# Kernel tuning notes

Hardware: AMD Instinct MI355X
Metric: run time of the kernel (lower is better)

The kernel has to match this reference:

```python
import jax, jax.numpy as jnp
import numpy as np

N_NODES = 100000
N_EDGES = 1600000
D_FEAT = 48


def setup_inputs() -> dict:
    key = jax.random.key(0)
    k1, k2, k3, k4 = jax.random.split(key, 4)
    rows = jax.random.randint(k1, (N_EDGES,), 0, N_NODES, dtype=jnp.int32)
    cols = jax.random.randint(k2, (N_EDGES,), 0, N_NODES, dtype=jnp.int32)
    vals = jax.random.uniform(k3, (N_EDGES,), dtype=jnp.float32)
    embeds = jax.random.normal(k4, (N_NODES, D_FEAT), dtype=jnp.float32)
    return {"rows": rows, "cols": cols, "vals": vals, "embeds": embeds}


def reference(rows, cols, vals, embeds):
    # out = spmm(adj, embeds): out[r] = sum_{e: rows[e]==r} vals[e] * embeds[cols[e]]
    msgs = vals[:, None] * embeds[cols]  # [E, d] gather + scale
    out = jax.ops.segment_sum(msgs, rows, num_segments=embeds.shape[0])  # [N, d]
    return out
```

## Files before the change

kernel.cpp:

```cpp
#include <hip/hip_runtime.h>
#include <hip/hip_fp16.h>


#define N_NODES 100000
#define N_EDGES 1600000
#define D_FEAT  48

#define RPB 128
#define NBUCKETS ((N_NODES + RPB - 1) / RPB)
#define NWG 256
#define CHUNK ((N_EDGES + NWG - 1) / NWG)
#define MAT (NBUCKETS * NWG)
#define SCAN_CHUNK 1024
#define NB_SCAN ((MAT + SCAN_CHUNK - 1) / SCAN_CHUNK)
#define CONV_N4 ((N_NODES * D_FEAT) / 4)
#define CONV_BLK ((CONV_N4 + 1023) / 1024)
#define CAP 3072

__global__ __launch_bounds__(1024) void count_convert(const int* __restrict__ rows,
                                                      unsigned int* __restrict__ mat,
                                                      const float4* __restrict__ esrc,
                                                      __half2* __restrict__ edst) {
    const int t = threadIdx.x;
    if (blockIdx.x < NWG) {
        __shared__ unsigned int lc[NBUCKETS];
        const int w = blockIdx.x;
        for (int i = t; i < NBUCKETS; i += 1024) lc[i] = 0u;
        __syncthreads();
        const int lo = w * CHUNK;
        const int hi = (lo + CHUNK < N_EDGES) ? lo + CHUNK : N_EDGES;
        for (int e = lo + t; e < hi; e += 1024)
            atomicAdd(&lc[((unsigned)rows[e]) >> 7], 1u);
        __syncthreads();
        for (int b = t; b < NBUCKETS; b += 1024)
            mat[b * NWG + w] = lc[b];
    } else {
        int i = (blockIdx.x - NWG) * 1024 + t;
        if (i < CONV_N4) {
            float4 v = esrc[i];
            edst[2 * i]     = __floats2half2_rn(v.x, v.y);
            edst[2 * i + 1] = __floats2half2_rn(v.z, v.w);
        }
    }
}

__global__ __launch_bounds__(256) void scan_phase1(const unsigned int* __restrict__ mat,
                                                   unsigned int* __restrict__ bsum) {
    __shared__ unsigned int s[256];
    const int blk = blockIdx.x, t = threadIdx.x;
    const int base = blk * SCAN_CHUNK + t * 4;
    unsigned int sum = 0;
#pragma unroll
    for (int k = 0; k < 4; ++k) {
        int i = base + k;
        if (i < MAT) sum += mat[i];
    }
    s[t] = sum;
    __syncthreads();
    for (int off = 128; off > 0; off >>= 1) {
        if (t < off) s[t] += s[t + off];
        __syncthreads();
    }
    if (t == 0) bsum[blk] = s[0];
}

__global__ __launch_bounds__(256) void scan_phase3(unsigned int* __restrict__ mat,
                                                   const unsigned int* __restrict__ bsum,
                                                   unsigned int* __restrict__ bstart) {
    __shared__ unsigned int s[256];
    __shared__ unsigned int bpre[256];
    const int blk = blockIdx.x, t = threadIdx.x;
    bpre[t] = (t < NB_SCAN) ? bsum[t] : 0u;
    __syncthreads();
    for (int off = 1; off < 256; off <<= 1) {
        unsigned int u = (t >= off) ? bpre[t - off] : 0u;
        __syncthreads();
        bpre[t] += u;
        __syncthreads();
    }
    const unsigned int blkbase = (blk == 0) ? 0u : bpre[blk - 1];

    const int base = blk * SCAN_CHUNK + t * 4;
    unsigned int c[4];
    unsigned int sum = 0;
#pragma unroll
    for (int k = 0; k < 4; ++k) {
        int i = base + k;
        c[k] = (i < MAT) ? mat[i] : 0u;
        sum += c[k];
    }
    s[t] = sum;
    __syncthreads();
    for (int off = 1; off < 256; off <<= 1) {
        unsigned int u = (t >= off) ? s[t - off] : 0u;
        __syncthreads();
        s[t] += u;
        __syncthreads();
    }
    unsigned int prefix = blkbase + ((t == 0) ? 0u : s[t - 1]);
#pragma unroll
    for (int k = 0; k < 4; ++k) {
        int i = base + k;
        if (i < MAT) {
            mat[i] = prefix;
            if ((i & (NWG - 1)) == 0) bstart[i >> 8] = prefix;
            prefix += c[k];
        }
    }
    if (blk == 0 && t == 0) bstart[NBUCKETS] = N_EDGES;
}

__global__ __launch_bounds__(1024) void place_kernel(const int* __restrict__ rows,
                                                     const int* __restrict__ cols,
                                                     const float* __restrict__ vals,
                                                     const unsigned int* __restrict__ mat,
                                                     int2* __restrict__ buf1) {
    __shared__ unsigned int lc[NBUCKETS];
    const int w = blockIdx.x, t = threadIdx.x;
    for (int b = t; b < NBUCKETS; b += 1024) lc[b] = mat[b * NWG + w];
    __syncthreads();
    const int lo = w * CHUNK;
    const int hi = (lo + CHUNK < N_EDGES) ? lo + CHUNK : N_EDGES;
    for (int e = lo + t; e < hi; e += 1024) {
        unsigned r = (unsigned)rows[e];
        unsigned c = (unsigned)cols[e];
        unsigned int pos = atomicAdd(&lc[r >> 7], 1u);
        unsigned hv = (unsigned)__half_as_ushort(__float2half_rn(vals[e]));
        buf1[pos] = make_int2((int)(((r & 127u) << 17) | c),
                              (int)((hv << 17) | c));
    }
}

__global__ __launch_bounds__(512) void finalize_spmm(const unsigned int* __restrict__ bstart,
                                                     const int2* __restrict__ buf1,
                                                     const __half2* __restrict__ embeds_h2,
                                                     float* __restrict__ out) {
    __shared__ unsigned int sedge[CAP];
    __shared__ unsigned int rstart[RPB + 1];
    __shared__ unsigned int rc[RPB];
    __shared__ unsigned int wtot[2];
    const int b = blockIdx.x, t = threadIdx.x;
    const unsigned int S = bstart[b];
    const unsigned int E = bstart[b + 1];
    const unsigned int cnt = E - S;
    const int g   = t >> 5;
    const int sub = t & 31;
    const bool act = sub < 24;
    const int row0 = b * RPB;

#define PROC(q)                                                       \
    {                                                                 \
        union { __half h; unsigned short u; } hv;                     \
        hv.u = (unsigned short)((q) >> 17);                           \
        float vv = __half2float(hv.h);                                \
        __half2 e2v = embeds_h2[((q) & 0x1FFFFu) * 24 + sub];         \
        ax = fmaf(vv, __low2float(e2v), ax);                          \
        ay = fmaf(vv, __high2float(e2v), ay);                         \
    }

    if (t < RPB) rc[t] = 0u;
    __syncthreads();
    for (unsigned int k = S + t; k < E; k += 512)
        atomicAdd(&rc[(unsigned)buf1[k].x >> 17], 1u);
    __syncthreads();
    unsigned int myc = 0, inc = 0;
    if (t < RPB) {
        myc = rc[t];
        inc = myc;
#pragma unroll
        for (int off = 1; off < 64; off <<= 1) {
            unsigned int u = __shfl_up(inc, off, 64);
            if ((t & 63) >= off) inc += u;
        }
        if ((t & 63) == 63) wtot[t >> 6] = inc;
    }
    __syncthreads();
    if (t < RPB) {
        if (t >= 64) inc += wtot[0];
        unsigned int pre = inc - myc;
        rstart[t] = pre;
        rc[t] = pre;
    }
    if (t == 0) rstart[RPB] = cnt;
    __syncthreads();

    if (cnt <= CAP) {
        for (unsigned int k = S + t; k < E; k += 512) {
            int2 cv = buf1[k];
            unsigned int pos = atomicAdd(&rc[(unsigned)cv.x >> 17], 1u);
            sedge[pos] = (unsigned int)cv.y;
        }
        __syncthreads();

        for (int rr = g * 8; rr < g * 8 + 8; ++rr) {
            int row = row0 + rr;
            if (row >= N_NODES) break;
            unsigned int j = rstart[rr], end = rstart[rr + 1];
            float ax = 0.f, ay = 0.f;
            for (; j + 8 <= end; j += 8) {
                unsigned int q0 = sedge[j + 0];
                unsigned int q1 = sedge[j + 1];
                unsigned int q2 = sedge[j + 2];
                unsigned int q3 = sedge[j + 3];
                unsigned int q4 = sedge[j + 4];
                unsigned int q5 = sedge[j + 5];
                unsigned int q6 = sedge[j + 6];
                unsigned int q7 = sedge[j + 7];
                if (act) {
                    PROC(q0) PROC(q1) PROC(q2) PROC(q3)
                    PROC(q4) PROC(q5) PROC(q6) PROC(q7)
                }
            }
            for (; j < end; ++j) {
                unsigned int q = sedge[j];
                if (act) PROC(q)
            }
            if (act)
                *(float2*)(out + (size_t)row * D_FEAT + sub * 2) = make_float2(ax, ay);
        }
    } else {
        for (int rr = g * 8; rr < g * 8 + 8; ++rr) {
            int row = row0 + rr;
            if (row >= N_NODES) break;
            float ax = 0.f, ay = 0.f;
            for (unsigned int k = S; k < E; ++k) {
                int2 cv = buf1[k];
                if (((unsigned)cv.x >> 17) == (unsigned)rr && act) {
                    unsigned int q = (unsigned int)cv.y;
                    PROC(q)
                }
            }
            if (act)
                *(float2*)(out + (size_t)row * D_FEAT + sub * 2) = make_float2(ax, ay);
        }
    }
#undef PROC
}

__global__ __launch_bounds__(256) void zero_out_kernel(float4* __restrict__ out, int n4) {
    int i = blockIdx.x * 256 + threadIdx.x;
    if (i < n4) out[i] = make_float4(0.f, 0.f, 0.f, 0.f);
}
__global__ __launch_bounds__(256) void spmm_atomic_kernel(const int* __restrict__ rows,
                                                          const int* __restrict__ cols,
                                                          const float* __restrict__ vals,
                                                          const float* __restrict__ embeds,
                                                          float* __restrict__ out) {
    long long tid = (long long)blockIdx.x * 256 + threadIdx.x;
    const long long total = (long long)N_EDGES * 12;
    if (tid >= total) return;
    int e = (int)(tid / 12), q = (int)(tid % 12);
    int r = rows[e], c = cols[e];
    float v = vals[e];
    const float4 emb = *(const float4*)(embeds + (long long)c * D_FEAT + q * 4);
    float* o = out + (long long)r * D_FEAT + q * 4;
    atomicAdd(o + 0, v * emb.x);
    atomicAdd(o + 1, v * emb.y);
    atomicAdd(o + 2, v * emb.z);
    atomicAdd(o + 3, v * emb.w);
}

extern "C" void kernel_launch(void* const* d_in, const int* in_sizes, int n_in,
                              void* d_out, int out_size, void* d_ws, size_t ws_size,
                              hipStream_t stream) {
    const int*   rows   = (const int*)d_in[0];
    const int*   cols   = (const int*)d_in[1];
    const float* vals   = (const float*)d_in[2];
    const float* embeds = (const float*)d_in[3];
    float*       out    = (float*)d_out;

    unsigned int* mat = (unsigned int*)d_ws;
    size_t mat_bytes  = ((size_t)MAT * 4 + 15) & ~(size_t)15;
    unsigned int* bstart = (unsigned int*)((char*)d_ws + mat_bytes);
    size_t bs_bytes   = (((size_t)(NBUCKETS + 1) * 4) + 15) & ~(size_t)15;
    unsigned int* bsum = (unsigned int*)((char*)d_ws + mat_bytes + bs_bytes);
    size_t bsum_bytes = (((size_t)NB_SCAN * 4) + 15) & ~(size_t)15;
    int2* buf1 = (int2*)((char*)d_ws + mat_bytes + bs_bytes + bsum_bytes);
    __half2* embeds_h2 = (__half2*)((char*)buf1 + (size_t)N_EDGES * 8);
    size_t need = mat_bytes + bs_bytes + bsum_bytes +
                  (size_t)N_EDGES * 8 + (size_t)N_NODES * D_FEAT * 2;

    if (ws_size < need) {
        int n4 = out_size / 4;
        zero_out_kernel<<<(n4 + 255) / 256, 256, 0, stream>>>((float4*)out, n4);
        long long total = (long long)N_EDGES * 12;
        spmm_atomic_kernel<<<(int)((total + 255) / 256), 256, 0, stream>>>(rows, cols, vals, embeds, out);
        return;
    }

    count_convert<<<NWG + CONV_BLK, 1024, 0, stream>>>(rows, mat,
                                                       (const float4*)embeds, embeds_h2);
    scan_phase1<<<NB_SCAN, 256, 0, stream>>>(mat, bsum);
    scan_phase3<<<NB_SCAN, 256, 0, stream>>>(mat, bsum, bstart);
    place_kernel<<<NWG, 1024, 0, stream>>>(rows, cols, vals, mat, buf1);
    finalize_spmm<<<NBUCKETS, 512, 0, stream>>>(bstart, buf1, embeds_h2, out);
}
```

Baseline: 78.47 us.

## Quantize embeddings to int8 with per-row fp16 scale folded into edge values

```diff
diff --git a/kernel.cpp b/kernel.cpp
--- a/kernel.cpp
+++ b/kernel.cpp
@@ -13,14 +13,15 @@
 #define MAT (NBUCKETS * NWG)
 #define SCAN_CHUNK 1024
 #define NB_SCAN ((MAT + SCAN_CHUNK - 1) / SCAN_CHUNK)
-#define CONV_N4 ((N_NODES * D_FEAT) / 4)
-#define CONV_BLK ((CONV_N4 + 1023) / 1024)
+#define QROWS_PER_BLK 16
+#define QBLK (N_NODES / QROWS_PER_BLK)
 #define CAP 3072
 
 __global__ __launch_bounds__(1024) void count_convert(const int* __restrict__ rows,
                                                       unsigned int* __restrict__ mat,
-                                                      const float4* __restrict__ esrc,
-                                                      __half2* __restrict__ edst) {
+                                                      const float2* __restrict__ esrc,
+                                                      unsigned short* __restrict__ embq,
+                                                      __half* __restrict__ scale_h) {
     const int t = threadIdx.x;
     if (blockIdx.x < NWG) {
         __shared__ unsigned int lc[NBUCKETS];
@@ -35,11 +36,24 @@
         for (int b = t; b < NBUCKETS; b += 1024)
             mat[b * NWG + w] = lc[b];
     } else {
-        int i = (blockIdx.x - NWG) * 1024 + t;
-        if (i < CONV_N4) {
-            float4 v = esrc[i];
-            edst[2 * i]     = __floats2half2_rn(v.x, v.y);
-            edst[2 * i + 1] = __floats2half2_rn(v.z, v.w);
+        const int row  = (blockIdx.x - NWG) * QROWS_PER_BLK + (t >> 6);
+        const int lane = t & 63;
+        if (row < N_NODES) {
+            float2 v = make_float2(0.f, 0.f);
+            if (lane < 24) v = esrc[(size_t)row * 24 + lane];
+            float m = fmaxf(fabsf(v.x), fabsf(v.y));
+#pragma unroll
+            for (int mask = 1; mask <= 32; mask <<= 1)
+                m = fmaxf(m, __shfl_xor(m, mask));
+            float inv = (m > 0.f) ? 127.f / m : 0.f;
+            if (lane < 24) {
+                int lo8 = __float2int_rn(v.x * inv);
+                int hi8 = __float2int_rn(v.y * inv);
+                embq[(size_t)row * 32 + lane] =
+                    (unsigned short)((lo8 & 0xff) | ((hi8 & 0xff) << 8));
+            }
+            if (lane == 24)
+                scale_h[row] = __float2half(m * (1.f / 127.f));
         }
     }
 }
@@ -113,6 +127,7 @@
 __global__ __launch_bounds__(1024) void place_kernel(const int* __restrict__ rows,
                                                      const int* __restrict__ cols,
                                                      const float* __restrict__ vals,
+                                                     const __half* __restrict__ scale_h,
                                                      const unsigned int* __restrict__ mat,
                                                      int2* __restrict__ buf1) {
     __shared__ unsigned int lc[NBUCKETS];
@@ -125,7 +140,8 @@
         unsigned r = (unsigned)rows[e];
         unsigned c = (unsigned)cols[e];
         unsigned int pos = atomicAdd(&lc[r >> 7], 1u);
-        unsigned hv = (unsigned)__half_as_ushort(__float2half_rn(vals[e]));
+        float vs = vals[e] * __half2float(scale_h[c]);
+        unsigned hv = (unsigned)__half_as_ushort(__float2half_rn(vs));
         buf1[pos] = make_int2((int)(((r & 127u) << 17) | c),
                               (int)((hv << 17) | c));
     }
@@ -133,7 +149,7 @@
 
 __global__ __launch_bounds__(512) void finalize_spmm(const unsigned int* __restrict__ bstart,
                                                      const int2* __restrict__ buf1,
-                                                     const __half2* __restrict__ embeds_h2,
+                                                     const unsigned short* __restrict__ embq,
                                                      float* __restrict__ out) {
     __shared__ unsigned int sedge[CAP];
     __shared__ unsigned int rstart[RPB + 1];
@@ -148,14 +164,12 @@
     const bool act = sub < 24;
     const int row0 = b * RPB;
 
-#define PROC(q)                                                       \
-    {                                                                 \
-        union { __half h; unsigned short u; } hv;                     \
-        hv.u = (unsigned short)((q) >> 17);                           \
-        float vv = __half2float(hv.h);                                \
-        __half2 e2v = embeds_h2[((q) & 0x1FFFFu) * 24 + sub];         \
-        ax = fmaf(vv, __low2float(e2v), ax);                          \
-        ay = fmaf(vv, __high2float(e2v), ay);                         \
+#define PROC(q)                                                          \
+    {                                                                    \
+        unsigned short qq = embq[(((q) & 0x1FFFFu) << 5) + sub];         \
+        float vs = __half2float(__ushort_as_half((unsigned short)((q) >> 17))); \
+        ax = fmaf(vs, (float)(int)(signed char)(qq & 0xff), ax);         \
+        ay = fmaf(vs, (float)(int)(signed char)(qq >> 8), ay);           \
     }
 
     if (t < RPB) rc[t] = 0u;
@@ -276,9 +290,12 @@
     unsigned int* bsum = (unsigned int*)((char*)d_ws + mat_bytes + bs_bytes);
     size_t bsum_bytes = (((size_t)NB_SCAN * 4) + 15) & ~(size_t)15;
     int2* buf1 = (int2*)((char*)d_ws + mat_bytes + bs_bytes + bsum_bytes);
-    __half2* embeds_h2 = (__half2*)((char*)buf1 + (size_t)N_EDGES * 8);
-    size_t need = mat_bytes + bs_bytes + bsum_bytes +
-                  (size_t)N_EDGES * 8 + (size_t)N_NODES * D_FEAT * 2;
+    size_t buf1_bytes = (size_t)N_EDGES * 8;
+    unsigned short* embq = (unsigned short*)((char*)buf1 + buf1_bytes);
+    size_t embq_bytes = (size_t)N_NODES * 64;
+    __half* scale_h = (__half*)((char*)embq + embq_bytes);
+    size_t need = mat_bytes + bs_bytes + bsum_bytes + buf1_bytes + embq_bytes +
+                  (size_t)N_NODES * 2;
 
     if (ws_size < need) {
         int n4 = out_size / 4;
@@ -288,10 +305,10 @@
         return;
     }
 
-    count_convert<<<NWG + CONV_BLK, 1024, 0, stream>>>(rows, mat,
-                                                       (const float4*)embeds, embeds_h2);
+    count_convert<<<NWG + QBLK, 1024, 0, stream>>>(rows, mat, (const float2*)embeds,
+                                                   embq, scale_h);
     scan_phase1<<<NB_SCAN, 256, 0, stream>>>(mat, bsum);
     scan_phase3<<<NB_SCAN, 256, 0, stream>>>(mat, bsum, bstart);
-    place_kernel<<<NWG, 1024, 0, stream>>>(rows, cols, vals, mat, buf1);
-    finalize_spmm<<<NBUCKETS, 512, 0, stream>>>(bstart, buf1, embeds_h2, out);
-}
+    place_kernel<<<NWG, 1024, 0, stream>>>(rows, cols, vals, scale_h, mat, buf1);
+    finalize_spmm<<<NBUCKETS, 512, 0, stream>>>(bstart, buf1, embq, out);
+}
```

New measurement: 92.05 us. +17.3%, slower.

## Replace two-pass global scan with atomic bucket offsets and in-block prefix scan

Applied to the files above, without the earlier changes.

```diff
diff --git a/kernel.cpp b/kernel.cpp
--- a/kernel.cpp
+++ b/kernel.cpp
@@ -10,15 +10,13 @@
 #define NBUCKETS ((N_NODES + RPB - 1) / RPB)
 #define NWG 256
 #define CHUNK ((N_EDGES + NWG - 1) / NWG)
-#define MAT (NBUCKETS * NWG)
-#define SCAN_CHUNK 1024
-#define NB_SCAN ((MAT + SCAN_CHUNK - 1) / SCAN_CHUNK)
 #define CONV_N4 ((N_NODES * D_FEAT) / 4)
 #define CONV_BLK ((CONV_N4 + 1023) / 1024)
 #define CAP 3072
 
 __global__ __launch_bounds__(1024) void count_convert(const int* __restrict__ rows,
                                                       unsigned int* __restrict__ mat,
+                                                      unsigned int* __restrict__ btot,
                                                       const float4* __restrict__ esrc,
                                                       __half2* __restrict__ edst) {
     const int t = threadIdx.x;
@@ -32,8 +30,10 @@
         for (int e = lo + t; e < hi; e += 1024)
             atomicAdd(&lc[((unsigned)rows[e]) >> 7], 1u);
         __syncthreads();
-        for (int b = t; b < NBUCKETS; b += 1024)
-            mat[b * NWG + w] = lc[b];
+        for (int b = t; b < NBUCKETS; b += 1024) {
+            unsigned int c = lc[b];
+            if (c) mat[(size_t)b * NWG + w] = atomicAdd(&btot[b], c);
+        }
     } else {
         int i = (blockIdx.x - NWG) * 1024 + t;
         if (i < CONV_N4) {
@@ -44,81 +44,33 @@
     }
 }
 
-__global__ __launch_bounds__(256) void scan_phase1(const unsigned int* __restrict__ mat,
-                                                   unsigned int* __restrict__ bsum) {
-    __shared__ unsigned int s[256];
-    const int blk = blockIdx.x, t = threadIdx.x;
-    const int base = blk * SCAN_CHUNK + t * 4;
-    unsigned int sum = 0;
-#pragma unroll
-    for (int k = 0; k < 4; ++k) {
-        int i = base + k;
-        if (i < MAT) sum += mat[i];
-    }
-    s[t] = sum;
-    __syncthreads();
-    for (int off = 128; off > 0; off >>= 1) {
-        if (t < off) s[t] += s[t + off];
-        __syncthreads();
-    }
-    if (t == 0) bsum[blk] = s[0];
-}
-
-__global__ __launch_bounds__(256) void scan_phase3(unsigned int* __restrict__ mat,
-                                                   const unsigned int* __restrict__ bsum,
-                                                   unsigned int* __restrict__ bstart) {
-    __shared__ unsigned int s[256];
-    __shared__ unsigned int bpre[256];
-    const int blk = blockIdx.x, t = threadIdx.x;
-    bpre[t] = (t < NB_SCAN) ? bsum[t] : 0u;
-    __syncthreads();
-    for (int off = 1; off < 256; off <<= 1) {
-        unsigned int u = (t >= off) ? bpre[t - off] : 0u;
-        __syncthreads();
-        bpre[t] += u;
-        __syncthreads();
-    }
-    const unsigned int blkbase = (blk == 0) ? 0u : bpre[blk - 1];
-
-    const int base = blk * SCAN_CHUNK + t * 4;
-    unsigned int c[4];
-    unsigned int sum = 0;
-#pragma unroll
-    for (int k = 0; k < 4; ++k) {
-        int i = base + k;
-        c[k] = (i < MAT) ? mat[i] : 0u;
-        sum += c[k];
-    }
-    s[t] = sum;
-    __syncthreads();
-    for (int off = 1; off < 256; off <<= 1) {
-        unsigned int u = (t >= off) ? s[t - off] : 0u;
-        __syncthreads();
-        s[t] += u;
-        __syncthreads();
-    }
-    unsigned int prefix = blkbase + ((t == 0) ? 0u : s[t - 1]);
-#pragma unroll
-    for (int k = 0; k < 4; ++k) {
-        int i = base + k;
-        if (i < MAT) {
-            mat[i] = prefix;
-            if ((i & (NWG - 1)) == 0) bstart[i >> 8] = prefix;
-            prefix += c[k];
-        }
-    }
-    if (blk == 0 && t == 0) bstart[NBUCKETS] = N_EDGES;
-}
-
 __global__ __launch_bounds__(1024) void place_kernel(const int* __restrict__ rows,
                                                      const int* __restrict__ cols,
                                                      const float* __restrict__ vals,
                                                      const unsigned int* __restrict__ mat,
+                                                     const unsigned int* __restrict__ btot,
+                                                     unsigned int* __restrict__ bstart,
                                                      int2* __restrict__ buf1) {
     __shared__ unsigned int lc[NBUCKETS];
+    __shared__ unsigned int sc[1024];
     const int w = blockIdx.x, t = threadIdx.x;
-    for (int b = t; b < NBUCKETS; b += 1024) lc[b] = mat[b * NWG + w];
-    __syncthreads();
+    unsigned int v = (t < NBUCKETS) ? btot[t] : 0u;
+    sc[t] = v;
+    __syncthreads();
+    for (int off = 1; off < 1024; off <<= 1) {
+        unsigned int u = (t >= off) ? sc[t - off] : 0u;
+        __syncthreads();
+        sc[t] += u;
+        __syncthreads();
+    }
+    unsigned int pre = (t == 0) ? 0u : sc[t - 1];
+    if (t < NBUCKETS) {
+        lc[t] = pre + mat[(size_t)t * NWG + w];
+        if (w == 0) bstart[t] = pre;
+    }
+    if (w == 0 && t == 0) bstart[NBUCKETS] = N_EDGES;
+    __syncthreads();
+
     const int lo = w * CHUNK;
     const int hi = (lo + CHUNK < N_EDGES) ? lo + CHUNK : N_EDGES;
     for (int e = lo + t; e < hi; e += 1024) {
@@ -270,14 +222,14 @@
     float*       out    = (float*)d_out;
 
     unsigned int* mat = (unsigned int*)d_ws;
-    size_t mat_bytes  = ((size_t)MAT * 4 + 15) & ~(size_t)15;
-    unsigned int* bstart = (unsigned int*)((char*)d_ws + mat_bytes);
+    size_t mat_bytes  = ((size_t)NBUCKETS * NWG * 4 + 15) & ~(size_t)15;
+    unsigned int* btot = (unsigned int*)((char*)d_ws + mat_bytes);
+    size_t btot_bytes = (((size_t)NBUCKETS * 4) + 15) & ~(size_t)15;
+    unsigned int* bstart = (unsigned int*)((char*)btot + btot_bytes);
     size_t bs_bytes   = (((size_t)(NBUCKETS + 1) * 4) + 15) & ~(size_t)15;
-    unsigned int* bsum = (unsigned int*)((char*)d_ws + mat_bytes + bs_bytes);
-    size_t bsum_bytes = (((size_t)NB_SCAN * 4) + 15) & ~(size_t)15;
-    int2* buf1 = (int2*)((char*)d_ws + mat_bytes + bs_bytes + bsum_bytes);
+    int2* buf1 = (int2*)((char*)bstart + bs_bytes);
     __half2* embeds_h2 = (__half2*)((char*)buf1 + (size_t)N_EDGES * 8);
-    size_t need = mat_bytes + bs_bytes + bsum_bytes +
+    size_t need = mat_bytes + btot_bytes + bs_bytes +
                   (size_t)N_EDGES * 8 + (size_t)N_NODES * D_FEAT * 2;
 
     if (ws_size < need) {
@@ -288,10 +240,9 @@
         return;
     }
 
-    count_convert<<<NWG + CONV_BLK, 1024, 0, stream>>>(rows, mat,
+    hipMemsetAsync(btot, 0, (size_t)NBUCKETS * 4, stream);
+    count_convert<<<NWG + CONV_BLK, 1024, 0, stream>>>(rows, mat, btot,
                                                        (const float4*)embeds, embeds_h2);
-    scan_phase1<<<NB_SCAN, 256, 0, stream>>>(mat, bsum);
-    scan_phase3<<<NB_SCAN, 256, 0, stream>>>(mat, bsum, bstart);
-    place_kernel<<<NWG, 1024, 0, stream>>>(rows, cols, vals, mat, buf1);
+    place_kernel<<<NWG, 1024, 0, stream>>>(rows, cols, vals, mat, btot, bstart, buf1);
     finalize_spmm<<<NBUCKETS, 512, 0, stream>>>(bstart, buf1, embeds_h2, out);
 }
```

After: 81.79 us. 4.2% more time.
